# Optimization experiments

Hardware: AMD Instinct MI355X
Metric: run time of the kernel (lower is better)

The kernel has to match this reference:

```python
import jax, jax.numpy as jnp
import numpy as np

N_NODES = 50000
N_EDGES = 800000
IN_SIZE, HID_SIZE, OUT_SIZE = 512, 128, 64


def _graph_conv(feat, src, dst, W, b, out_norm, in_norm, activation=None):
    # DGL GraphConv with norm='both': h' = D_in^{-1/2} A D_out^{-1/2} (X W) + b
    x = feat * out_norm[:, None]          # scale by source (out-degree) norm
    x = x @ W                             # dense transform first (in >= out)
    msg = x[src]                          # gather per-edge messages [E, d]
    agg = jax.ops.segment_sum(msg, dst, num_segments=N_NODES)
    h = agg * in_norm[:, None] + b
    if activation is not None:
        h = activation(h)
    return h


def setup_inputs() -> dict:
    key = jax.random.key(0)
    k1, k2, k3, k4, k5, k6, k7 = jax.random.split(key, 7)
    features = jax.random.normal(k1, (N_NODES, IN_SIZE), dtype=jnp.float32)
    src = jax.random.randint(k2, (N_EDGES,), 0, N_NODES, dtype=jnp.int64)
    dst = jax.random.randint(k3, (N_EDGES,), 0, N_NODES, dtype=jnp.int64)
    # Glorot-style init as in dglnn.GraphConv
    W1 = jax.random.normal(k4, (IN_SIZE, HID_SIZE), dtype=jnp.float32) * (1.0 / np.sqrt(IN_SIZE))
    b1 = jnp.zeros((HID_SIZE,), dtype=jnp.float32)
    W2 = jax.random.normal(k5, (HID_SIZE, OUT_SIZE), dtype=jnp.float32) * (1.0 / np.sqrt(HID_SIZE))
    b2 = jnp.zeros((OUT_SIZE,), dtype=jnp.float32)
    return {"features": features, "W1": W1, "b1": b1, "W2": W2, "b2": b2,
            "src": src, "dst": dst}


def reference(features, W1, b1, W2, b2, src, dst):
    ones = jnp.ones((N_EDGES,), dtype=features.dtype)
    out_deg = jax.ops.segment_sum(ones, src, num_segments=N_NODES)
    in_deg = jax.ops.segment_sum(ones, dst, num_segments=N_NODES)
    out_norm = jax.lax.rsqrt(jnp.clip(out_deg, 1.0))  # deg clamped to >=1 as in DGL
    in_norm = jax.lax.rsqrt(jnp.clip(in_deg, 1.0))
    h = _graph_conv(features, src, dst, W1, b1, out_norm, in_norm, activation=jax.nn.relu)
    # dropout omitted (eval mode)
    h = _graph_conv(h, src, dst, W2, b2, out_norm, in_norm, activation=None)
    return h
```

## Files before the change

kernel.cpp:

```cpp
#include <hip/hip_runtime.h>

#define N_NODES 50000
#define IN_SIZE 512
#define HID 128
#define OUT 64
#define NB 256
#define SHIFT 7
#define NBUCK 391

typedef _Float16 f16x8 __attribute__((ext_vector_type(8)));
typedef _Float16 f16x2 __attribute__((ext_vector_type(2)));
typedef float    f32x4 __attribute__((ext_vector_type(4)));

__global__ void k_detect(const int* __restrict__ p, int* __restrict__ flag) {
    if (threadIdx.x == 0 && blockIdx.x == 0) {
        int odd_zero = 1;
        for (int i = 1; i < 129; i += 2) {
            if (p[i] != 0) { odd_zero = 0; break; }
        }
        *flag = odd_zero;
    }
}

__device__ __forceinline__ int load_idx(const void* p, int e, bool w) {
    return w ? (int)((const long long*)p)[e] : ((const int*)p)[e];
}

__global__ __launch_bounds__(256) void k_chist(const void* __restrict__ dstp,
                                               const int* __restrict__ flag,
                                               int* __restrict__ hist, int E, int EPB) {
    __shared__ int bins[NBUCK];
    const int t = threadIdx.x, b = blockIdx.x;
    for (int i = t; i < NBUCK; i += 256) bins[i] = 0;
    __syncthreads();
    bool w = (*flag) != 0;
    int eend = min(E, (b + 1) * EPB);
    for (int e = b * EPB + t; e < eend; e += 256)
        atomicAdd(&bins[load_idx(dstp, e, w) >> SHIFT], 1);
    __syncthreads();
    for (int i = t; i < NBUCK; i += 256) hist[i * NB + b] = bins[i];
}

__global__ __launch_bounds__(256) void k_scanA(int* __restrict__ hist, int* __restrict__ bsum) {
    __shared__ int s[256];
    const int t = threadIdx.x, g = blockIdx.x;
    int v = hist[g * NB + t];
    s[t] = v;
    __syncthreads();
    for (int off = 1; off < 256; off <<= 1) {
        int u = (t >= off) ? s[t - off] : 0;
        __syncthreads();
        s[t] += u;
        __syncthreads();
    }
    hist[g * NB + t] = s[t] - v;
    if (t == 255) bsum[g] = s[255];
}

__global__ __launch_bounds__(512) void k_scanB(const int* __restrict__ bsum, int* __restrict__ bb) {
    __shared__ int s[512];
    const int t = threadIdx.x;
    int v = (t < NBUCK) ? bsum[t] : 0;
    s[t] = v;
    __syncthreads();
    for (int off = 1; off < 512; off <<= 1) {
        int u = (t >= off) ? s[t - off] : 0;
        __syncthreads();
        s[t] += u;
        __syncthreads();
    }
    if (t <= NBUCK) bb[t] = s[t] - v;
}

__global__ __launch_bounds__(256) void k_scanC(int* __restrict__ hist, const int* __restrict__ bb) {
    const int t = threadIdx.x, g = blockIdx.x;
    hist[g * NB + t] += bb[g];
}

__global__ __launch_bounds__(256) void k_cscatter(const void* __restrict__ srcp,
                                                  const void* __restrict__ dstp,
                                                  const int* __restrict__ flag,
                                                  const int* __restrict__ hist,
                                                  int* __restrict__ tmp_src,
                                                  unsigned char* __restrict__ tmp_dl,
                                                  int* __restrict__ cnt_out,
                                                  int E, int EPB) {
    __shared__ int cur[NBUCK];
    const int t = threadIdx.x, b = blockIdx.x;
    for (int i = t; i < NBUCK; i += 256) cur[i] = hist[i * NB + b];
    __syncthreads();
    bool w = (*flag) != 0;
    int eend = min(E, (b + 1) * EPB);
    for (int e = b * EPB + t; e < eend; e += 256) {
        int s = load_idx(srcp, e, w);
        int d = load_idx(dstp, e, w);
        atomicAdd(&cnt_out[s], 1);
        int pos = atomicAdd(&cur[d >> SHIFT], 1);
        tmp_src[pos] = s;
        tmp_dl[pos]  = (unsigned char)(d & 127);
    }
}

__global__ __launch_bounds__(256) void k_fine(const int* __restrict__ tmp_src,
                                              const unsigned char* __restrict__ tmp_dl,
                                              const int* __restrict__ bb,
                                              const int* __restrict__ cnt_out,
                                              int* __restrict__ rp,
                                              int* __restrict__ esrc,
                                              float* __restrict__ innorm,
                                              float* __restrict__ onorm) {
    __shared__ int fcnt[128];
    __shared__ int sc[128];
    __shared__ int fcur[128];
    const int t = threadIdx.x, u = blockIdx.x;
    const int e0 = bb[u], e1 = bb[u + 1];
    if (t < 128) fcnt[t] = 0;
    __syncthreads();
    for (int e = e0 + t; e < e1; e += 256)
        atomicAdd(&fcnt[tmp_dl[e]], 1);
    __syncthreads();
    if (t < 128) sc[t] = fcnt[t];
    __syncthreads();
    for (int off = 1; off < 128; off <<= 1) {
        int v = (t < 128 && t >= off) ? sc[t - off] : 0;
        __syncthreads();
        if (t < 128) sc[t] += v;
        __syncthreads();
    }
    if (t < 128) {
        int base = e0 + sc[t] - fcnt[t];
        fcur[t] = base;
        int node = u * 128 + t;
        if (node < N_NODES) {
            rp[node] = base;
            int c = fcnt[t]; if (c < 1) c = 1;
            innorm[node] = 1.0f / sqrtf((float)c);
            int a = cnt_out[node]; if (a < 1) a = 1;
            onorm[node] = 1.0f / sqrtf((float)a);
        }
    }
    if (u == NBUCK - 1 && t == 0) rp[N_NODES] = e1;
    __syncthreads();
    for (int e = e0 + t; e < e1; e += 256) {
        int pos = atomicAdd(&fcur[tmp_dl[e]], 1);
        esrc[pos] = tmp_src[e];
    }
}

__global__ __launch_bounds__(256) void k_wt(const float* __restrict__ W1, _Float16* __restrict__ W1T,
                                            const float* __restrict__ W2, _Float16* __restrict__ W2T) {
    int i = blockIdx.x * 256 + threadIdx.x;
    if (i < IN_SIZE * HID) {
        int k = i >> 7, n = i & (HID - 1);
        W1T[(size_t)n * IN_SIZE + k] = (_Float16)W1[i];
    } else {
        int j = i - IN_SIZE * HID;
        if (j < HID * OUT) {
            int k = j >> 6, n = j & (OUT - 1);
            W2T[(size_t)n * HID + k] = (_Float16)W2[j];
        }
    }
}

#define LDA 40
__global__ __launch_bounds__(256) void k_gemm1_mfma(const float* __restrict__ A,
                                                    const _Float16* __restrict__ BT,
                                                    const float* __restrict__ onorm,
                                                    _Float16* __restrict__ X) {
    __shared__ _Float16 As[64 * LDA];
    __shared__ _Float16 Bs[128 * LDA];
    const int tid  = threadIdx.x;
    const int wave = tid >> 6, lane = tid & 63;
    const int lm = lane & 15, lq = lane >> 4;
    const int row0 = blockIdx.x * 64;

    const int ar = tid >> 2, aq = tid & 3;
    int arow = row0 + ar; if (arow >= N_NODES) arow = N_NODES - 1;
    const float* aptr = A + (size_t)arow * IN_SIZE + aq * 8;
    _Float16* asd = &As[ar * LDA + aq * 8];
    const int bn = tid >> 1, bh = tid & 1;
    const _Float16* bptr = BT + (size_t)bn * IN_SIZE + bh * 16;
    _Float16* bsd = &Bs[bn * LDA + bh * 16];

    f32x4 acc[8];
#pragma unroll
    for (int nt = 0; nt < 8; ++nt) acc[nt] = (f32x4){0.f, 0.f, 0.f, 0.f};

    for (int k0 = 0; k0 < IN_SIZE; k0 += 32) {
        float4 a0 = *(const float4*)(aptr + k0);
        float4 a1 = *(const float4*)(aptr + k0 + 4);
        f16x8  b0 = *(const f16x8*)(bptr + k0);
        f16x8  b1 = *(const f16x8*)(bptr + k0 + 8);
        f16x8 ap = {(_Float16)a0.x, (_Float16)a0.y, (_Float16)a0.z, (_Float16)a0.w,
                    (_Float16)a1.x, (_Float16)a1.y, (_Float16)a1.z, (_Float16)a1.w};
        __syncthreads();
        *(f16x8*)asd       = ap;
        *(f16x8*)bsd       = b0;
        *(f16x8*)(bsd + 8) = b1;
        __syncthreads();
        f16x8 af = *(const f16x8*)&As[(wave * 16 + lm) * LDA + lq * 8];
#pragma unroll
        for (int nt = 0; nt < 8; ++nt) {
            f16x8 bf = *(const f16x8*)&Bs[(nt * 16 + lm) * LDA + lq * 8];
            acc[nt] = __builtin_amdgcn_mfma_f32_16x16x32_f16(af, bf, acc[nt], 0, 0, 0);
        }
    }
#pragma unroll
    for (int i = 0; i < 4; ++i) {
        int row = row0 + wave * 16 + lq * 4 + i;
        if (row < N_NODES) {
            float on = onorm[row];
            _Float16* o = X + (size_t)row * HID + lm;
#pragma unroll
            for (int nt = 0; nt < 8; ++nt)
                o[nt * 16] = (_Float16)(acc[nt][i] * on);
        }
    }
}

__global__ __launch_bounds__(256) void k_agg1(const _Float16* __restrict__ X, const int* __restrict__ rp,
                                              const int* __restrict__ esrc, const float* __restrict__ innorm,
                                              const float* __restrict__ onorm, const float* __restrict__ b1,
                                              _Float16* __restrict__ H) {
    const int n = blockIdx.x * 4 + (threadIdx.x >> 6);
    const int c = (threadIdx.x & 63) << 1;
    if (n >= N_NODES) return;
    const int e0 = rp[n], e1 = rp[n + 1];
    float a0 = 0.f, a1 = 0.f;
    int e = e0;
    for (; e + 3 < e1; e += 4) {
        int s0 = esrc[e], s1 = esrc[e + 1], s2 = esrc[e + 2], s3 = esrc[e + 3];
        f16x2 v0 = *(const f16x2*)&X[(size_t)s0 * HID + c];
        f16x2 v1 = *(const f16x2*)&X[(size_t)s1 * HID + c];
        f16x2 v2 = *(const f16x2*)&X[(size_t)s2 * HID + c];
        f16x2 v3 = *(const f16x2*)&X[(size_t)s3 * HID + c];
        a0 += ((float)v0.x + (float)v1.x) + ((float)v2.x + (float)v3.x);
        a1 += ((float)v0.y + (float)v1.y) + ((float)v2.y + (float)v3.y);
    }
    for (; e < e1; ++e) {
        f16x2 v = *(const f16x2*)&X[(size_t)esrc[e] * HID + c];
        a0 += (float)v.x; a1 += (float)v.y;
    }
    float inn = innorm[n], on = onorm[n];
    float2 b = *(const float2*)&b1[c];
    float h0 = fmaxf(a0 * inn + b.x, 0.f) * on;
    float h1 = fmaxf(a1 * inn + b.y, 0.f) * on;
    *(f16x2*)&H[(size_t)n * HID + c] = (f16x2){(_Float16)h0, (_Float16)h1};
}

#define LDK 136
__global__ __launch_bounds__(256) void k_gemm2_mfma(const _Float16* __restrict__ Hm,
                                                    const _Float16* __restrict__ W2T,
                                                    _Float16* __restrict__ X2) {
    __shared__ _Float16 Hs[64 * LDK];
    __shared__ _Float16 Ws[64 * LDK];
    const int tid  = threadIdx.x;
    const int wave = tid >> 6, lane = tid & 63;
    const int lm = lane & 15, lq = lane >> 4;
    const int row0 = blockIdx.x * 64;

    const int r = tid >> 2, cch = (tid & 3) * 32;
    int hrow = row0 + r; if (hrow >= N_NODES) hrow = N_NODES - 1;
    const _Float16* hp = Hm + (size_t)hrow * HID + cch;
    const _Float16* wp = W2T + (size_t)r * HID + cch;
    _Float16* hd = &Hs[r * LDK + cch];
    _Float16* wd = &Ws[r * LDK + cch];
#pragma unroll
    for (int i = 0; i < 4; ++i) {
        *(f16x8*)(hd + i * 8) = *(const f16x8*)(hp + i * 8);
        *(f16x8*)(wd + i * 8) = *(const f16x8*)(wp + i * 8);
    }
    __syncthreads();

    f32x4 acc[4];
#pragma unroll
    for (int nt = 0; nt < 4; ++nt) acc[nt] = (f32x4){0.f, 0.f, 0.f, 0.f};
#pragma unroll
    for (int k0 = 0; k0 < HID; k0 += 32) {
        f16x8 af = *(const f16x8*)&Hs[(wave * 16 + lm) * LDK + k0 + lq * 8];
#pragma unroll
        for (int nt = 0; nt < 4; ++nt) {
            f16x8 bf = *(const f16x8*)&Ws[(nt * 16 + lm) * LDK + k0 + lq * 8];
            acc[nt] = __builtin_amdgcn_mfma_f32_16x16x32_f16(af, bf, acc[nt], 0, 0, 0);
        }
    }
#pragma unroll
    for (int i = 0; i < 4; ++i) {
        int row = row0 + wave * 16 + lq * 4 + i;
        if (row < N_NODES) {
            _Float16* o = X2 + (size_t)row * OUT + lm;
#pragma unroll
            for (int nt = 0; nt < 4; ++nt)
                o[nt * 16] = (_Float16)acc[nt][i];
        }
    }
}

__global__ __launch_bounds__(256) void k_agg2(const _Float16* __restrict__ X2, const int* __restrict__ rp,
                                              const int* __restrict__ esrc, const float* __restrict__ innorm,
                                              const float* __restrict__ b2, float* __restrict__ out) {
    const int n = blockIdx.x * 8 + (threadIdx.x >> 5);
    const int c = (threadIdx.x & 31) << 1;
    if (n >= N_NODES) return;
    const int e0 = rp[n], e1 = rp[n + 1];
    float a0 = 0.f, a1 = 0.f;
    int e = e0;
    for (; e + 3 < e1; e += 4) {
        int s0 = esrc[e], s1 = esrc[e + 1], s2 = esrc[e + 2], s3 = esrc[e + 3];
        f16x2 v0 = *(const f16x2*)&X2[(size_t)s0 * OUT + c];
        f16x2 v1 = *(const f16x2*)&X2[(size_t)s1 * OUT + c];
        f16x2 v2 = *(const f16x2*)&X2[(size_t)s2 * OUT + c];
        f16x2 v3 = *(const f16x2*)&X2[(size_t)s3 * OUT + c];
        a0 += ((float)v0.x + (float)v1.x) + ((float)v2.x + (float)v3.x);
        a1 += ((float)v0.y + (float)v1.y) + ((float)v2.y + (float)v3.y);
    }
    for (; e < e1; ++e) {
        f16x2 v = *(const f16x2*)&X2[(size_t)esrc[e] * OUT + c];
        a0 += (float)v.x; a1 += (float)v.y;
    }
    float inn = innorm[n];
    float2 b = *(const float2*)&b2[c];
    *(float2*)&out[(size_t)n * OUT + c] = make_float2(a0 * inn + b.x, a1 * inn + b.y);
}

extern "C" void kernel_launch(void* const* d_in, const int* in_sizes, int n_in,
                              void* d_out, int out_size, void* d_ws, size_t ws_size,
                              hipStream_t stream) {
    const float* feat = (const float*)d_in[0];
    const float* W1   = (const float*)d_in[1];
    const float* b1   = (const float*)d_in[2];
    const float* W2   = (const float*)d_in[3];
    const float* b2   = (const float*)d_in[4];
    const void*  srcp = (const void*)d_in[5];
    const void*  dstp = (const void*)d_in[6];
    const int    E    = in_sizes[5];
    float* out = (float*)d_out;

    char* w = (char*)d_ws;
    size_t off = 0;
    auto alloc = [&](size_t bytes) -> void* {
        off = (off + 255) & ~(size_t)255;
        void* p = w + off;
        off += bytes;
        return p;
    };
    int*   cnt_out = (int*)alloc((size_t)N_NODES * 4);
    int*   hist    = (int*)alloc((size_t)NBUCK * NB * 4);
    int*   bsum    = (int*)alloc((size_t)NBUCK * 4);
    int*   bb      = (int*)alloc((size_t)(NBUCK + 1) * 4);
    int*   rp      = (int*)alloc((size_t)(N_NODES + 1) * 4);
    int*   flag    = (int*)alloc(4);
    int*   tmp_src = (int*)alloc((size_t)E * 4);
    unsigned char* tmp_dl = (unsigned char*)alloc((size_t)E);
    int*   esrc    = (int*)alloc((size_t)E * 4);
    float* onorm   = (float*)alloc((size_t)N_NODES * 4);
    float* innorm  = (float*)alloc((size_t)N_NODES * 4);
    _Float16* W1T  = (_Float16*)alloc((size_t)IN_SIZE * HID * 2);
    _Float16* W2T  = (_Float16*)alloc((size_t)HID * OUT * 2);
    _Float16* X1   = (_Float16*)alloc((size_t)N_NODES * HID * 2);
    _Float16* Hbuf = (_Float16*)alloc((size_t)N_NODES * HID * 2);
    _Float16* X2   = (_Float16*)alloc((size_t)N_NODES * OUT * 2);
    (void)ws_size; (void)n_in; (void)out_size;

    const int EPB = (E + NB - 1) / NB;

    hipMemsetAsync(cnt_out, 0, (size_t)N_NODES * 4, stream);
    k_detect<<<1, 64, 0, stream>>>((const int*)dstp, flag);

    k_chist<<<NB, 256, 0, stream>>>(dstp, flag, hist, E, EPB);
    k_scanA<<<NBUCK, 256, 0, stream>>>(hist, bsum);
    k_scanB<<<1, 512, 0, stream>>>(bsum, bb);
    k_scanC<<<NBUCK, 256, 0, stream>>>(hist, bb);
    k_cscatter<<<NB, 256, 0, stream>>>(srcp, dstp, flag, hist, tmp_src, tmp_dl, cnt_out, E, EPB);
    k_fine<<<NBUCK, 256, 0, stream>>>(tmp_src, tmp_dl, bb, cnt_out, rp, esrc, innorm, onorm);

    k_wt<<<(IN_SIZE * HID + HID * OUT + 255) / 256, 256, 0, stream>>>(W1, W1T, W2, W2T);

    k_gemm1_mfma<<<(N_NODES + 63) / 64, 256, 0, stream>>>(feat, W1T, onorm, X1);
    k_agg1<<<(N_NODES + 3) / 4, 256, 0, stream>>>(X1, rp, esrc, innorm, onorm, b1, Hbuf);
    k_gemm2_mfma<<<(N_NODES + 63) / 64, 256, 0, stream>>>(Hbuf, W2T, X2);
    k_agg2<<<(N_NODES + 7) / 8, 256, 0, stream>>>(X2, rp, esrc, innorm, b2, out);
}
```

Before: 323.4 us.

## Replace global out-degree atomics with shared-memory packed source histogram; fuse small kernels

The out-degree count moves out of the scatter kernel, where it used global atomics, into a dedicated histogram kernel. That kernel packs two 16-bit counters per 32-bit shared-memory word, and a separate reduction kernel then builds onorm. The index-width detection is inlined into each kernel as a wave ballot, the weight transpose is folded into the coarse histogram launch, and the scanC pass is merged into cscatter. Together these drop the memset and three launches but add a 6.4 MB partial-histogram buffer. The 16-bit counters rely on each block seeing fewer than 65536 hits per node, which holds for these inputs.

```diff
diff --git a/kernel.cpp b/kernel.cpp
--- a/kernel.cpp
+++ b/kernel.cpp
@@ -7,38 +7,88 @@
 #define NB 256
 #define SHIFT 7
 #define NBUCK 391
+#define SB 64
+#define NBINS32 25000
 
 typedef _Float16 f16x8 __attribute__((ext_vector_type(8)));
 typedef _Float16 f16x2 __attribute__((ext_vector_type(2)));
 typedef float    f32x4 __attribute__((ext_vector_type(4)));
 
-__global__ void k_detect(const int* __restrict__ p, int* __restrict__ flag) {
-    if (threadIdx.x == 0 && blockIdx.x == 0) {
-        int odd_zero = 1;
-        for (int i = 1; i < 129; i += 2) {
-            if (p[i] != 0) { odd_zero = 0; break; }
-        }
-        *flag = odd_zero;
-    }
+__device__ __forceinline__ bool detect_w(const int* p, int t, int* sh) {
+    if (t < 64) {
+        unsigned long long m = __ballot(p[2 * t + 1] == 0);
+        if (t == 0) *sh = (m == ~0ull) ? 1 : 0;
+    }
+    __syncthreads();
+    return *sh != 0;
 }
 
 __device__ __forceinline__ int load_idx(const void* p, int e, bool w) {
     return w ? (int)((const long long*)p)[e] : ((const int*)p)[e];
 }
 
-__global__ __launch_bounds__(256) void k_chist(const void* __restrict__ dstp,
-                                               const int* __restrict__ flag,
-                                               int* __restrict__ hist, int E, int EPB) {
+__global__ __launch_bounds__(256) void k_chist_wt(const void* __restrict__ dstp,
+                                                  int* __restrict__ hist, int E, int EPB,
+                                                  const float* __restrict__ W1, _Float16* __restrict__ W1T,
+                                                  const float* __restrict__ W2, _Float16* __restrict__ W2T) {
+    const int t = threadIdx.x, b = blockIdx.x;
+    if (b >= NB) {
+        int i = (b - NB) * 256 + t;
+        if (i < IN_SIZE * HID) {
+            int k = i >> 7, n = i & (HID - 1);
+            W1T[(size_t)n * IN_SIZE + k] = (_Float16)W1[i];
+        } else {
+            int j = i - IN_SIZE * HID;
+            if (j < HID * OUT) {
+                int k = j >> 6, n = j & (OUT - 1);
+                W2T[(size_t)n * HID + k] = (_Float16)W2[j];
+            }
+        }
+        return;
+    }
     __shared__ int bins[NBUCK];
-    const int t = threadIdx.x, b = blockIdx.x;
+    __shared__ int shw;
     for (int i = t; i < NBUCK; i += 256) bins[i] = 0;
-    __syncthreads();
-    bool w = (*flag) != 0;
+    bool w = detect_w((const int*)dstp, t, &shw);
+    __syncthreads();
     int eend = min(E, (b + 1) * EPB);
     for (int e = b * EPB + t; e < eend; e += 256)
         atomicAdd(&bins[load_idx(dstp, e, w) >> SHIFT], 1);
     __syncthreads();
     for (int i = t; i < NBUCK; i += 256) hist[i * NB + b] = bins[i];
+}
+
+__global__ __launch_bounds__(256) void k_srchist(const void* __restrict__ srcp,
+                                                 unsigned int* __restrict__ partial, int E, int ESB) {
+    __shared__ unsigned int bins[NBINS32];
+    __shared__ int shw;
+    const int t = threadIdx.x, b = blockIdx.x;
+    for (int i = t; i < NBINS32; i += 256) bins[i] = 0;
+    bool w = detect_w((const int*)srcp, t, &shw);
+    __syncthreads();
+    int eend = min(E, (b + 1) * ESB);
+    for (int e = b * ESB + t; e < eend; e += 256) {
+        int s = load_idx(srcp, e, w);
+        atomicAdd(&bins[s >> 1], 1u << ((s & 1) << 4));
+    }
+    __syncthreads();
+    for (int i = t; i < NBINS32; i += 256) partial[(size_t)b * NBINS32 + i] = bins[i];
+}
+
+__global__ __launch_bounds__(256) void k_sred(const unsigned int* __restrict__ partial,
+                                              float* __restrict__ onorm) {
+    int wd = blockIdx.x * 256 + threadIdx.x;
+    if (wd >= NBINS32) return;
+    int c0 = 0, c1 = 0;
+    for (int b = 0; b < SB; ++b) {
+        unsigned int v = partial[(size_t)b * NBINS32 + wd];
+        c0 += (int)(v & 0xFFFFu);
+        c1 += (int)(v >> 16);
+    }
+    if (c0 < 1) c0 = 1;
+    if (c1 < 1) c1 = 1;
+    onorm[2 * wd]     = 1.0f / sqrtf((float)c0);
+    onorm[2 * wd + 1] = 1.0f / sqrtf((float)c1);
 }
 
 __global__ __launch_bounds__(256) void k_scanA(int* __restrict__ hist, int* __restrict__ bsum) {
@@ -72,29 +122,23 @@
     if (t <= NBUCK) bb[t] = s[t] - v;
 }
 
-__global__ __launch_bounds__(256) void k_scanC(int* __restrict__ hist, const int* __restrict__ bb) {
-    const int t = threadIdx.x, g = blockIdx.x;
-    hist[g * NB + t] += bb[g];
-}
-
 __global__ __launch_bounds__(256) void k_cscatter(const void* __restrict__ srcp,
                                                   const void* __restrict__ dstp,
-                                                  const int* __restrict__ flag,
                                                   const int* __restrict__ hist,
+                                                  const int* __restrict__ bb,
                                                   int* __restrict__ tmp_src,
                                                   unsigned char* __restrict__ tmp_dl,
-                                                  int* __restrict__ cnt_out,
                                                   int E, int EPB) {
     __shared__ int cur[NBUCK];
+    __shared__ int shw;
     const int t = threadIdx.x, b = blockIdx.x;
-    for (int i = t; i < NBUCK; i += 256) cur[i] = hist[i * NB + b];
-    __syncthreads();
-    bool w = (*flag) != 0;
+    for (int i = t; i < NBUCK; i += 256) cur[i] = hist[i * NB + b] + bb[i];
+    bool w = detect_w((const int*)dstp, t, &shw);
+    __syncthreads();
     int eend = min(E, (b + 1) * EPB);
     for (int e = b * EPB + t; e < eend; e += 256) {
         int s = load_idx(srcp, e, w);
         int d = load_idx(dstp, e, w);
-        atomicAdd(&cnt_out[s], 1);
         int pos = atomicAdd(&cur[d >> SHIFT], 1);
         tmp_src[pos] = s;
         tmp_dl[pos]  = (unsigned char)(d & 127);
@@ -104,11 +148,9 @@
 __global__ __launch_bounds__(256) void k_fine(const int* __restrict__ tmp_src,
                                               const unsigned char* __restrict__ tmp_dl,
                                               const int* __restrict__ bb,
-                                              const int* __restrict__ cnt_out,
                                               int* __restrict__ rp,
                                               int* __restrict__ esrc,
-                                              float* __restrict__ innorm,
-                                              float* __restrict__ onorm) {
+                                              float* __restrict__ innorm) {
     __shared__ int fcnt[128];
     __shared__ int sc[128];
     __shared__ int fcur[128];
@@ -135,8 +177,6 @@
             rp[node] = base;
             int c = fcnt[t]; if (c < 1) c = 1;
             innorm[node] = 1.0f / sqrtf((float)c);
-            int a = cnt_out[node]; if (a < 1) a = 1;
-            onorm[node] = 1.0f / sqrtf((float)a);
         }
     }
     if (u == NBUCK - 1 && t == 0) rp[N_NODES] = e1;
@@ -144,21 +184,6 @@
     for (int e = e0 + t; e < e1; e += 256) {
         int pos = atomicAdd(&fcur[tmp_dl[e]], 1);
         esrc[pos] = tmp_src[e];
-    }
-}
-
-__global__ __launch_bounds__(256) void k_wt(const float* __restrict__ W1, _Float16* __restrict__ W1T,
-                                            const float* __restrict__ W2, _Float16* __restrict__ W2T) {
-    int i = blockIdx.x * 256 + threadIdx.x;
-    if (i < IN_SIZE * HID) {
-        int k = i >> 7, n = i & (HID - 1);
-        W1T[(size_t)n * IN_SIZE + k] = (_Float16)W1[i];
-    } else {
-        int j = i - IN_SIZE * HID;
-        if (j < HID * OUT) {
-            int k = j >> 6, n = j & (OUT - 1);
-            W2T[(size_t)n * HID + k] = (_Float16)W2[j];
-        }
     }
 }
 
@@ -344,12 +369,11 @@
         off += bytes;
         return p;
     };
-    int*   cnt_out = (int*)alloc((size_t)N_NODES * 4);
     int*   hist    = (int*)alloc((size_t)NBUCK * NB * 4);
     int*   bsum    = (int*)alloc((size_t)NBUCK * 4);
     int*   bb      = (int*)alloc((size_t)(NBUCK + 1) * 4);
     int*   rp      = (int*)alloc((size_t)(N_NODES + 1) * 4);
-    int*   flag    = (int*)alloc(4);
+    unsigned int* spart = (unsigned int*)alloc((size_t)SB * NBINS32 * 4);
     int*   tmp_src = (int*)alloc((size_t)E * 4);
     unsigned char* tmp_dl = (unsigned char*)alloc((size_t)E);
     int*   esrc    = (int*)alloc((size_t)E * 4);
@@ -363,18 +387,16 @@
     (void)ws_size; (void)n_in; (void)out_size;
 
     const int EPB = (E + NB - 1) / NB;
-
-    hipMemsetAsync(cnt_out, 0, (size_t)N_NODES * 4, stream);
-    k_detect<<<1, 64, 0, stream>>>((const int*)dstp, flag);
-
-    k_chist<<<NB, 256, 0, stream>>>(dstp, flag, hist, E, EPB);
+    const int ESB = (E + SB - 1) / SB;
+    const int WTB = (IN_SIZE * HID + HID * OUT + 255) / 256;
+
+    k_chist_wt<<<NB + WTB, 256, 0, stream>>>(dstp, hist, E, EPB, W1, W1T, W2, W2T);
+    k_srchist<<<SB, 256, 0, stream>>>(srcp, spart, E, ESB);
+    k_sred<<<(NBINS32 + 255) / 256, 256, 0, stream>>>(spart, onorm);
     k_scanA<<<NBUCK, 256, 0, stream>>>(hist, bsum);
     k_scanB<<<1, 512, 0, stream>>>(bsum, bb);
-    k_scanC<<<NBUCK, 256, 0, stream>>>(hist, bb);
-    k_cscatter<<<NB, 256, 0, stream>>>(srcp, dstp, flag, hist, tmp_src, tmp_dl, cnt_out, E, EPB);
-    k_fine<<<NBUCK, 256, 0, stream>>>(tmp_src, tmp_dl, bb, cnt_out, rp, esrc, innorm, onorm);
-
-    k_wt<<<(IN_SIZE * HID + HID * OUT + 255) / 256, 256, 0, stream>>>(W1, W1T, W2, W2T);
+    k_cscatter<<<NB, 256, 0, stream>>>(srcp, dstp, hist, bb, tmp_src, tmp_dl, E, EPB);
+    k_fine<<<NBUCK, 256, 0, stream>>>(tmp_src, tmp_dl, bb, rp, esrc, innorm);
 
     k_gemm1_mfma<<<(N_NODES + 63) / 64, 256, 0, stream>>>(feat, W1T, onorm, X1);
     k_agg1<<<(N_NODES + 3) / 4, 256, 0, stream>>>(X1, rp, esrc, innorm, onorm, b1, Hbuf);
```

New measurement: 316.6 us. -2.1%, faster.
